# Kernel tuning notes

Hardware: AMD Instinct MI355X
Metric: run time of the kernel (lower is better)

The kernel has to match this reference:

```python
import jax, jax.numpy as jnp
import numpy as np

F = 64      # input_v_size
E = 64      # emb_v_size
H = 8       # int(sqrt(emb_v_size))
P = 512     # proj_e_size
B, T = 64, 256


def setup_inputs() -> dict:
    key = jax.random.key(0)
    ks = jax.random.split(key, 14)
    s1 = 1.0            # Linear(1->H): fan_in=1
    s2 = 1.0 / np.sqrt(H)
    s3 = 1.0 / np.sqrt(F * E)
    return {
        "x":    jax.random.normal(ks[0], (B, T, F), dtype=jnp.float32),
        "time": jax.random.uniform(ks[1], (B, T, F), dtype=jnp.float32),
        # stacked per-feature Linear(1->H): weight [F,H], bias [F,H]
        "w1v": jax.random.uniform(ks[2], (F, H), jnp.float32, -s1, s1),
        "b1v": jax.random.uniform(ks[3], (F, H), jnp.float32, -s1, s1),
        # stacked per-feature Linear(H->E, bias=False): [F,H,E]
        "w2v": jax.random.uniform(ks[4], (F, H, E), jnp.float32, -s2, s2),
        "w1t": jax.random.uniform(ks[5], (F, H), jnp.float32, -s1, s1),
        "b1t": jax.random.uniform(ks[6], (F, H), jnp.float32, -s1, s1),
        "w2t": jax.random.uniform(ks[7], (F, H, E), jnp.float32, -s2, s2),
        # Wx, Wt: Linear(F*E -> P) stored as [F*E, P] (= torch weight.T)
        "wx":  jax.random.uniform(ks[8], (F * E, P), jnp.float32, -s3, s3),
        "bx":  jax.random.uniform(ks[9], (P,), jnp.float32, -s3, s3),
        "wt":  jax.random.uniform(ks[10], (F * E, P), jnp.float32, -s3, s3),
        "bt":  jax.random.uniform(ks[11], (P,), jnp.float32, -s3, s3),
    }


def _branch(inp, w1, b1, w2):
    # inp [B,T,F]; w1,b1 [F,H]; w2 [F,H,E]
    h = jnp.tanh(inp[..., None] * w1 + b1)          # [B,T,F,H]
    e = jnp.einsum("btfh,fhe->btfe", h, w2)          # [B,T,F,E]
    return e.reshape(*inp.shape[:2], -1)              # [B,T,F*E]


def reference(x, time, w1v, b1v, w2v, w1t, b1t, w2t, wx, bx, wt, bt):
    x_out = _branch(x, w1v, b1v, w2v)
    t_out = _branch(time, w1t, b1t, w2t)
    return (x_out @ wx + bx) + (t_out @ wt + bt)      # [B,T,P]
```

## Files before the change

kernel.cpp:

```cpp
#include <hip/hip_runtime.h>
#include <cstdint>
#include <cstddef>

#define FF 64
#define EE 64
#define HH 8
#define PP 512
#define MM 16384
#define KK 1024

typedef __bf16 bf16x8 __attribute__((ext_vector_type(8)));
typedef float  floatx4 __attribute__((ext_vector_type(4)));

__device__ __forceinline__ unsigned short f2bf(float f) {
    unsigned int u = __float_as_uint(f);
    u += 0x7FFFu + ((u >> 16) & 1u);
    return (unsigned short)(u >> 16);
}

__device__ __forceinline__ unsigned pack2(unsigned short a, unsigned short b) {
    return (unsigned)a | ((unsigned)b << 16);
}

__device__ __forceinline__ float fast_tanh(float x) {
    float e, r;
    asm("v_exp_f32 %0, %1" : "=v"(e) : "v"(x * 2.8853900817779268f));
    float d = e + 1.0f;
    asm("v_rcp_f32 %0, %1" : "=v"(r) : "v"(d));
    return __builtin_fmaf(-2.0f, r, 1.0f);
}

__device__ __forceinline__ void gl_lds16(const unsigned short* g, unsigned short* s) {
    __builtin_amdgcn_global_load_lds(
        (__attribute__((address_space(1))) void*)(void*)g,
        (__attribute__((address_space(3))) void*)s,
        16, 0, 0);
}

__global__ __launch_bounds__(256) void combine_kernel(
    const float* __restrict__ w2v, const float* __restrict__ w2t,
    const float* __restrict__ wx,  const float* __restrict__ wt,
    unsigned short* __restrict__ BmatT)
{
    const int tid = threadIdx.x;
    const int bid = blockIdx.x;
    const int br = bid >> 7;
    const int f  = (bid >> 1) & 63;
    const int nh = bid & 1;
    const float* __restrict__ w2 = br ? w2t : w2v;
    const float* __restrict__ W  = br ? wt  : wx;
    __shared__ float w2s[HH * EE];
    for (int i = tid; i < HH * EE; i += 256) w2s[i] = w2[f * HH * EE + i];
    __syncthreads();
    const int n = nh * 256 + tid;
    float acc[HH] = {0,0,0,0,0,0,0,0};
    const float* Wcol = W + (size_t)f * EE * PP + n;
    #pragma unroll 8
    for (int e = 0; e < EE; ++e) {
        const float wv = Wcol[(size_t)e * PP];
        #pragma unroll
        for (int h = 0; h < HH; ++h)
            acc[h] = __builtin_fmaf(w2s[h * EE + e], wv, acc[h]);
    }
    uint4 v;
    v.x = pack2(f2bf(acc[0]), f2bf(acc[1]));
    v.y = pack2(f2bf(acc[2]), f2bf(acc[3]));
    v.z = pack2(f2bf(acc[4]), f2bf(acc[5]));
    v.w = pack2(f2bf(acc[6]), f2bf(acc[7]));
    *reinterpret_cast<uint4*>(&BmatT[(size_t)n * KK + br * 512 + f * 8]) = v;
}

__global__ __launch_bounds__(256) void gemm_fused_kernel(
    const float* __restrict__ x,   const float* __restrict__ tmv,
    const float* __restrict__ w1v, const float* __restrict__ b1v,
    const float* __restrict__ w1t, const float* __restrict__ b1t,
    const unsigned short* __restrict__ Bt,
    const float* __restrict__ bx, const float* __restrict__ bt,
    float* __restrict__ out)
{
    __shared__ __align__(16) unsigned short As[128 * 64];
    __shared__ __align__(16) unsigned short Bs[128 * 64];
    __shared__ __align__(16) float w1s[2 * FF * HH];
    __shared__ __align__(16) float b1s[2 * FF * HH];

    const int tid  = threadIdx.x;
    const int wave = tid >> 6;
    const int lane = tid & 63;
    const int m0 = blockIdx.x * 128;
    const int n0 = blockIdx.y * 128;

    {
        const float4 wsrc = (tid < 128) ? reinterpret_cast<const float4*>(w1v)[tid]
                                        : reinterpret_cast<const float4*>(w1t)[tid - 128];
        const float4 bsrc = (tid < 128) ? reinterpret_cast<const float4*>(b1v)[tid]
                                        : reinterpret_cast<const float4*>(b1t)[tid - 128];
        reinterpret_cast<float4*>(w1s)[tid] = wsrc;
        reinterpret_cast<float4*>(b1s)[tid] = bsrc;
    }
    __syncthreads();

    const int wr = wave >> 1;
    const int wc = wave & 1;
    const int q   = lane >> 4;
    const int ml  = lane & 15;
    const int mlx = ml & 7;
    const int lr  = lane >> 3;
    const int lkg = ((lane & 7) ^ lr) * 8;
    const int fi  = tid & 7;
    const int g   = tid >> 3;

    floatx4 acc[4][4];
    #pragma unroll
    for (int i = 0; i < 4; ++i)
        #pragma unroll
        for (int j = 0; j < 4; ++j)
            acc[i][j] = (floatx4){0.f, 0.f, 0.f, 0.f};

    for (int k0 = 0; k0 < KK; k0 += 64) {
        const int br = k0 >> 9;
        const int f0 = (k0 >> 3) & 63;

        #pragma unroll
        for (int i = 0; i < 4; ++i) {
            const int seg = wave * 4 + i;
            gl_lds16(&Bt[(size_t)(n0 + seg * 8 + lr) * KK + k0 + lkg], &Bs[seg * 512]);
        }

        {
            const float* __restrict__ inp = br ? tmv : x;
            const int f = f0 + fi;
            const float4 wlo = reinterpret_cast<const float4*>(w1s)[br * 128 + f * 2];
            const float4 whi = reinterpret_cast<const float4*>(w1s)[br * 128 + f * 2 + 1];
            const float4 blo = reinterpret_cast<const float4*>(b1s)[br * 128 + f * 2];
            const float4 bhi = reinterpret_cast<const float4*>(b1s)[br * 128 + f * 2 + 1];
            float vals[4];
            #pragma unroll
            for (int j = 0; j < 4; ++j)
                vals[j] = inp[(size_t)(m0 + g + 32 * j) * FF + f];
            const int pchunk = (fi ^ (g & 7)) * 8;
            #pragma unroll
            for (int j = 0; j < 4; ++j) {
                const int r = g + 32 * j;
                const float val = vals[j];
                float hv[8];
                hv[0] = fast_tanh(__builtin_fmaf(val, wlo.x, blo.x));
                hv[1] = fast_tanh(__builtin_fmaf(val, wlo.y, blo.y));
                hv[2] = fast_tanh(__builtin_fmaf(val, wlo.z, blo.z));
                hv[3] = fast_tanh(__builtin_fmaf(val, wlo.w, blo.w));
                hv[4] = fast_tanh(__builtin_fmaf(val, whi.x, bhi.x));
                hv[5] = fast_tanh(__builtin_fmaf(val, whi.y, bhi.y));
                hv[6] = fast_tanh(__builtin_fmaf(val, whi.z, bhi.z));
                hv[7] = fast_tanh(__builtin_fmaf(val, whi.w, bhi.w));
                uint4 v;
                v.x = pack2(f2bf(hv[0]), f2bf(hv[1]));
                v.y = pack2(f2bf(hv[2]), f2bf(hv[3]));
                v.z = pack2(f2bf(hv[4]), f2bf(hv[5]));
                v.w = pack2(f2bf(hv[6]), f2bf(hv[7]));
                *reinterpret_cast<uint4*>(&As[r * 64 + pchunk]) = v;
            }
        }
        __syncthreads();

        #pragma unroll
        for (int kk = 0; kk < 64; kk += 32) {
            const int cl = (kk >> 3) + q;
            const int co = (cl ^ mlx) * 8;
            bf16x8 af[4], bfr[4];
            #pragma unroll
            for (int mt = 0; mt < 4; ++mt)
                af[mt] = *reinterpret_cast<const bf16x8*>(
                    &As[(wr * 64 + mt * 16 + ml) * 64 + co]);
            #pragma unroll
            for (int nt = 0; nt < 4; ++nt)
                bfr[nt] = *reinterpret_cast<const bf16x8*>(
                    &Bs[(wc * 64 + nt * 16 + ml) * 64 + co]);
            #pragma unroll
            for (int mt = 0; mt < 4; ++mt)
                #pragma unroll
                for (int nt = 0; nt < 4; ++nt)
                    acc[mt][nt] = __builtin_amdgcn_mfma_f32_16x16x32_bf16(
                        af[mt], bfr[nt], acc[mt][nt], 0, 0, 0);
        }
        __syncthreads();
    }

    #pragma unroll
    for (int nt = 0; nt < 4; ++nt) {
        const int n = n0 + wc * 64 + nt * 16 + ml;
        const float bias = bx[n] + bt[n];
        #pragma unroll
        for (int mt = 0; mt < 4; ++mt) {
            const int mb = m0 + wr * 64 + mt * 16 + q * 4;
            #pragma unroll
            for (int r = 0; r < 4; ++r)
                out[(size_t)(mb + r) * PP + n] = acc[mt][nt][r] + bias;
        }
    }
}

extern "C" void kernel_launch(void* const* d_in, const int* in_sizes, int n_in,
                              void* d_out, int out_size, void* d_ws, size_t ws_size,
                              hipStream_t stream)
{
    const float* x   = (const float*)d_in[0];
    const float* tmv = (const float*)d_in[1];
    const float* w1v = (const float*)d_in[2];
    const float* b1v = (const float*)d_in[3];
    const float* w2v = (const float*)d_in[4];
    const float* w1t = (const float*)d_in[5];
    const float* b1t = (const float*)d_in[6];
    const float* w2t = (const float*)d_in[7];
    const float* wx  = (const float*)d_in[8];
    const float* bx  = (const float*)d_in[9];
    const float* wt  = (const float*)d_in[10];
    const float* bt  = (const float*)d_in[11];
    float* out = (float*)d_out;

    unsigned short* Bws = (unsigned short*)d_ws;

    combine_kernel<<<256, 256, 0, stream>>>(w2v, w2t, wx, wt, Bws);
    gemm_fused_kernel<<<dim3(MM / 128, PP / 128), 256, 0, stream>>>(
        x, tmv, w1v, b1v, w1t, b1t, Bws, bx, bt, out);
}
```

Before: 141.7 us.

## Retile fused GEMM to 64x256 blocks with 512 threads and prescale tanh inputs

Changes the fused GEMM block tile from 128x128 with 4 waves to 64x256 with 8 waves, so each block covers the full N width in two column blocks. The tanh activation A-tile is now recomputed for only two N-blocks instead of four, halving the redundant per-element exp/rcp work. The tanh scale constant is also folded into the staged w1/b1 values in LDS, removing one multiply per activation. In exchange, each wave holds a smaller 2x4 MFMA tile, which lowers A-fragment reuse, and the larger block could reduce occupancy.

Measured after the change: 125.6 us. 1.13x faster.

```diff
diff --git a/kernel.cpp b/kernel.cpp
--- a/kernel.cpp
+++ b/kernel.cpp
@@ -22,9 +22,9 @@
     return (unsigned)a | ((unsigned)b << 16);
 }
 
-__device__ __forceinline__ float fast_tanh(float x) {
+__device__ __forceinline__ float fast_tanh_s(float t) {
     float e, r;
-    asm("v_exp_f32 %0, %1" : "=v"(e) : "v"(x * 2.8853900817779268f));
+    asm("v_exp_f32 %0, %1" : "=v"(e) : "v"(t));
     float d = e + 1.0f;
     asm("v_rcp_f32 %0, %1" : "=v"(r) : "v"(d));
     return __builtin_fmaf(-2.0f, r, 1.0f);
@@ -70,7 +70,7 @@
     *reinterpret_cast<uint4*>(&BmatT[(size_t)n * KK + br * 512 + f * 8]) = v;
 }
 
-__global__ __launch_bounds__(256) void gemm_fused_kernel(
+__global__ __launch_bounds__(512, 4) void gemm_fused_kernel(
     const float* __restrict__ x,   const float* __restrict__ tmv,
     const float* __restrict__ w1v, const float* __restrict__ b1v,
     const float* __restrict__ w1t, const float* __restrict__ b1t,
@@ -78,40 +78,44 @@
     const float* __restrict__ bx, const float* __restrict__ bt,
     float* __restrict__ out)
 {
-    __shared__ __align__(16) unsigned short As[128 * 64];
-    __shared__ __align__(16) unsigned short Bs[128 * 64];
+    __shared__ __align__(16) unsigned short As[64 * 64];
+    __shared__ __align__(16) unsigned short Bs[256 * 64];
     __shared__ __align__(16) float w1s[2 * FF * HH];
     __shared__ __align__(16) float b1s[2 * FF * HH];
 
     const int tid  = threadIdx.x;
     const int wave = tid >> 6;
     const int lane = tid & 63;
-    const int m0 = blockIdx.x * 128;
-    const int n0 = blockIdx.y * 128;
+    const int m0 = blockIdx.x * 64;
+    const int n0 = blockIdx.y * 256;
 
     {
-        const float4 wsrc = (tid < 128) ? reinterpret_cast<const float4*>(w1v)[tid]
-                                        : reinterpret_cast<const float4*>(w1t)[tid - 128];
-        const float4 bsrc = (tid < 128) ? reinterpret_cast<const float4*>(b1v)[tid]
-                                        : reinterpret_cast<const float4*>(b1t)[tid - 128];
-        reinterpret_cast<float4*>(w1s)[tid] = wsrc;
-        reinterpret_cast<float4*>(b1s)[tid] = bsrc;
+        const float c = 2.8853900817779268f;
+        #pragma unroll
+        for (int t = 0; t < 2; ++t) {
+            const int idx = tid + t * 512;
+            const int br  = idx >> 9;
+            const int rem = idx & 511;
+            w1s[idx] = (br ? w1t : w1v)[rem] * c;
+            b1s[idx] = (br ? b1t : b1v)[rem] * c;
+        }
     }
     __syncthreads();
 
-    const int wr = wave >> 1;
-    const int wc = wave & 1;
+    const int wm  = wave >> 2;
+    const int wn  = wave & 3;
     const int q   = lane >> 4;
     const int ml  = lane & 15;
     const int mlx = ml & 7;
     const int lr  = lane >> 3;
     const int lkg = ((lane & 7) ^ lr) * 8;
     const int fi  = tid & 7;
-    const int g   = tid >> 3;
-
-    floatx4 acc[4][4];
+    const int arow = tid >> 3;
+    const int pchunk = (fi ^ (arow & 7)) * 8;
+
+    floatx4 acc[2][4];
     #pragma unroll
-    for (int i = 0; i < 4; ++i)
+    for (int i = 0; i < 2; ++i)
         #pragma unroll
         for (int j = 0; j < 4; ++j)
             acc[i][j] = (floatx4){0.f, 0.f, 0.f, 0.f};
@@ -129,35 +133,26 @@
         {
             const float* __restrict__ inp = br ? tmv : x;
             const int f = f0 + fi;
+            const float val = inp[(size_t)(m0 + arow) * FF + f];
             const float4 wlo = reinterpret_cast<const float4*>(w1s)[br * 128 + f * 2];
             const float4 whi = reinterpret_cast<const float4*>(w1s)[br * 128 + f * 2 + 1];
             const float4 blo = reinterpret_cast<const float4*>(b1s)[br * 128 + f * 2];
             const float4 bhi = reinterpret_cast<const float4*>(b1s)[br * 128 + f * 2 + 1];
-            float vals[4];
-            #pragma unroll
-            for (int j = 0; j < 4; ++j)
-                vals[j] = inp[(size_t)(m0 + g + 32 * j) * FF + f];
-            const int pchunk = (fi ^ (g & 7)) * 8;
-            #pragma unroll
-            for (int j = 0; j < 4; ++j) {
-                const int r = g + 32 * j;
-                const float val = vals[j];
-                float hv[8];
-                hv[0] = fast_tanh(__builtin_fmaf(val, wlo.x, blo.x));
-                hv[1] = fast_tanh(__builtin_fmaf(val, wlo.y, blo.y));
-                hv[2] = fast_tanh(__builtin_fmaf(val, wlo.z, blo.z));
-                hv[3] = fast_tanh(__builtin_fmaf(val, wlo.w, blo.w));
-                hv[4] = fast_tanh(__builtin_fmaf(val, whi.x, bhi.x));
-                hv[5] = fast_tanh(__builtin_fmaf(val, whi.y, bhi.y));
-                hv[6] = fast_tanh(__builtin_fmaf(val, whi.z, bhi.z));
-                hv[7] = fast_tanh(__builtin_fmaf(val, whi.w, bhi.w));
-                uint4 v;
-                v.x = pack2(f2bf(hv[0]), f2bf(hv[1]));
-                v.y = pack2(f2bf(hv[2]), f2bf(hv[3]));
-                v.z = pack2(f2bf(hv[4]), f2bf(hv[5]));
-                v.w = pack2(f2bf(hv[6]), f2bf(hv[7]));
-                *reinterpret_cast<uint4*>(&As[r * 64 + pchunk]) = v;
-            }
+            float hv[8];
+            hv[0] = fast_tanh_s(__builtin_fmaf(val, wlo.x, blo.x));
+            hv[1] = fast_tanh_s(__builtin_fmaf(val, wlo.y, blo.y));
+            hv[2] = fast_tanh_s(__builtin_fmaf(val, wlo.z, blo.z));
+            hv[3] = fast_tanh_s(__builtin_fmaf(val, wlo.w, blo.w));
+            hv[4] = fast_tanh_s(__builtin_fmaf(val, whi.x, bhi.x));
+            hv[5] = fast_tanh_s(__builtin_fmaf(val, whi.y, bhi.y));
+            hv[6] = fast_tanh_s(__builtin_fmaf(val, whi.z, bhi.z));
+            hv[7] = fast_tanh_s(__builtin_fmaf(val, whi.w, bhi.w));
+            uint4 v;
+            v.x = pack2(f2bf(hv[0]), f2bf(hv[1]));
+            v.y = pack2(f2bf(hv[2]), f2bf(hv[3]));
+            v.z = pack2(f2bf(hv[4]), f2bf(hv[5]));
+            v.w = pack2(f2bf(hv[6]), f2bf(hv[7]));
+            *reinterpret_cast<uint4*>(&As[arow * 64 + pchunk]) = v;
         }
         __syncthreads();
 
@@ -165,17 +160,17 @@
         for (int kk = 0; kk < 64; kk += 32) {
             const int cl = (kk >> 3) + q;
             const int co = (cl ^ mlx) * 8;
-            bf16x8 af[4], bfr[4];
-            #pragma unroll
-            for (int mt = 0; mt < 4; ++mt)
+            bf16x8 af[2], bfr[4];
+            #pragma unroll
+            for (int mt = 0; mt < 2; ++mt)
                 af[mt] = *reinterpret_cast<const bf16x8*>(
-                    &As[(wr * 64 + mt * 16 + ml) * 64 + co]);
+                    &As[(wm * 32 + mt * 16 + ml) * 64 + co]);
             #pragma unroll
             for (int nt = 0; nt < 4; ++nt)
                 bfr[nt] = *reinterpret_cast<const bf16x8*>(
-                    &Bs[(wc * 64 + nt * 16 + ml) * 64 + co]);
-            #pragma unroll
-            for (int mt = 0; mt < 4; ++mt)
+                    &Bs[(wn * 64 + nt * 16 + ml) * 64 + co]);
+            #pragma unroll
+            for (int mt = 0; mt < 2; ++mt)
                 #pragma unroll
                 for (int nt = 0; nt < 4; ++nt)
                     acc[mt][nt] = __builtin_amdgcn_mfma_f32_16x16x32_bf16(
@@ -184,16 +179,21 @@
         __syncthreads();
     }
 
+    float bias[4];
     #pragma unroll
     for (int nt = 0; nt < 4; ++nt) {
-        const int n = n0 + wc * 64 + nt * 16 + ml;
-        const float bias = bx[n] + bt[n];
-        #pragma unroll
-        for (int mt = 0; mt < 4; ++mt) {
-            const int mb = m0 + wr * 64 + mt * 16 + q * 4;
-            #pragma unroll
-            for (int r = 0; r < 4; ++r)
-                out[(size_t)(mb + r) * PP + n] = acc[mt][nt][r] + bias;
+        const int n = n0 + wn * 64 + nt * 16 + ml;
+        bias[nt] = bx[n] + bt[n];
+    }
+    #pragma unroll
+    for (int mt = 0; mt < 2; ++mt) {
+        const int mb = m0 + wm * 32 + mt * 16 + q * 4;
+        #pragma unroll
+        for (int r = 0; r < 4; ++r) {
+            float* orow = out + (size_t)(mb + r) * PP + n0 + wn * 64 + ml;
+            #pragma unroll
+            for (int nt = 0; nt < 4; ++nt)
+                orow[nt * 16] = acc[mt][nt][r] + bias[nt];
         }
     }
 }
@@ -219,6 +219,6 @@
     unsigned short* Bws = (unsigned short*)d_ws;
 
     combine_kernel<<<256, 256, 0, stream>>>(w2v, w2t, wx, wt, Bws);
-    gemm_fused_kernel<<<dim3(MM / 128, PP / 128), 256, 0, stream>>>(
+    gemm_fused_kernel<<<dim3(MM / 64, PP / 256), 512, 0, stream>>>(
         x, tmv, w1v, b1v, w1t, b1t, Bws, bx, bt, out);
 }
```
